# Kernel tuning notes

Hardware: AMD Instinct MI355X
Metric: run time of the kernel (lower is better)

Reference implementation:

```python
import jax, jax.numpy as jnp
import numpy as np

MULTIPLIER_N_BITS = 8
EPS = 1e-8


def setup_inputs() -> dict:
    key = jax.random.key(0)
    k1, k2, k3 = jax.random.split(key, 3)
    B, H, W, C, K = 16, 56, 56, 256, 16
    x = jax.random.normal(k1, (B, H, W, C), dtype=jnp.float32)
    # per-channel positive scales, typical activation-range magnitudes
    scales = jax.random.uniform(k2, (C,), dtype=jnp.float32, minval=0.1, maxval=2.0)
    # cluster centers live in the signed int domain [-2^(n-1), 2^(n-1)-1] of the multiplier
    cluster_centers = jax.random.uniform(k3, (K,), dtype=jnp.float32, minval=-128.0, maxval=127.0)
    return {"x": x, "scales": scales, "cluster_centers": cluster_centers}


def reference(x, scales, cluster_centers):
    mult = 2.0 ** (MULTIPLIER_N_BITS - 1)  # 128
    centers = jnp.round(cluster_centers)  # [K]
    # int_quantization_with_scale: clip(data/(scale+eps)*2^(n-1), -2^(n-1), 2^(n-1)-1)
    t = jnp.clip(x / (scales + EPS) * mult, -mult, mult - 1.0)  # [B,H,W,C]
    # nearest-center assignment over K centers ([...,K] intermediate)
    idx = jnp.argmin(jnp.abs(t[..., None] - centers), axis=-1)  # [B,H,W,C] int
    c = centers[idx]  # gather-dequant
    return c / mult * scales  # broadcast per-channel rescale
```

## Files before the change

kernel.cpp:

```cpp
#include <hip/hip_runtime.h>

#define NK 16
#define E  4

typedef float f32x4 __attribute__((ext_vector_type(4)));

__device__ __forceinline__ float argmin16(float t, const float* cen) {
    float best = 3.4e38f;
    float bc = 0.0f;
#pragma unroll
    for (int k = 0; k < NK; ++k) {
        float d = fabsf(t - cen[k]);
        bool p = d < best;
        best = p ? d : best;
        bc   = p ? cen[k] : bc;
    }
    return bc;
}

__global__ __launch_bounds__(256) void lutfq_kernel(
    const f32x4* __restrict__ x,
    const float* __restrict__ scales,
    const float* __restrict__ centers,
    f32x4*       __restrict__ out,
    int n4)
{
    __shared__ float s_lut[512];

    const int tid = threadIdx.x;
    const int i0 = blockIdx.x * (256 * E) + tid;

    f32x4 v[E];
#pragma unroll
    for (int u = 0; u < E; ++u) {
        int i = i0 + u * 256;
        v[u] = (i < n4) ? x[i] : f32x4{0.f, 0.f, 0.f, 0.f};
    }

    float cen[NK];
#pragma unroll
    for (int k = 0; k < NK; ++k) cen[k] = rintf(centers[k]);

    const int c4 = (tid & 63) * 4;
    const f32x4 sv = *reinterpret_cast<const f32x4*>(&scales[c4]);
    float den[4], r256[4], so[4];
#pragma unroll
    for (int j = 0; j < 4; ++j) {
        den[j]  = sv[j] + 1e-8f;
        r256[j] = 256.0f / den[j];
        so[j]   = sv[j] * 0.0078125f;
    }

    for (int ub = tid; ub < 512; ub += 256) {
        float t;
        if (ub == 0)        t = -128.0f;
        else if (ub >= 510) t = 127.0f;
        else                t = 0.5f * (float)(ub - 256) + 0.25f;
        s_lut[ub] = argmin16(t, cen);
    }
    __syncthreads();

    auto process = [&](f32x4 xv) -> f32x4 {
        f32x4 r;
#pragma unroll
        for (int j = 0; j < 4; ++j) {
            float u2 = xv[j] * r256[j];
            u2 = fminf(fmaxf(u2, -256.0f), 254.0f);

            float fl   = floorf(u2);
            float frac = u2 - fl;
            int   ub   = (int)fl + 256;

            float c = s_lut[ub];

            bool band = (frac < 0x1p-12f) | (frac > 1.0f - 0x1p-12f);
            bool rail = (u2 == -256.0f) | (u2 == 254.0f);
            if (band && !rail) {
                float t = (xv[j] / den[j]) * 128.0f;
                t = fminf(fmaxf(t, -128.0f), 127.0f);
                c = argmin16(t, cen);
            }
            r[j] = c * so[j];
        }
        return r;
    };

#pragma unroll
    for (int u = 0; u < E; ++u) {
        int i = i0 + u * 256;
        f32x4 r = process(v[u]);
        if (i < n4) __builtin_nontemporal_store(r, &out[i]);
    }
}

extern "C" void kernel_launch(void* const* d_in, const int* in_sizes, int n_in,
                              void* d_out, int out_size, void* d_ws, size_t ws_size,
                              hipStream_t stream) {
    const float* x       = (const float*)d_in[0];
    const float* scales  = (const float*)d_in[1];
    const float* centers = (const float*)d_in[2];
    float* out = (float*)d_out;

    int n4 = out_size / 4;
    int per_block = 256 * E;
    int blocks = (n4 + per_block - 1) / per_block;

    lutfq_kernel<<<blocks, 256, 0, stream>>>(
        (const f32x4*)x, scales, centers, (f32x4*)out, n4);
}
```

Measured before the change: 21.31 us.

## Precompute LUT and per-channel constants in a prep kernel via workspace

```diff
diff --git a/kernel.cpp b/kernel.cpp
--- a/kernel.cpp
+++ b/kernel.cpp
@@ -1,9 +1,16 @@
 #include <hip/hip_runtime.h>
 
 #define NK 16
-#define E  4
+#define E  7
 
-typedef float f32x4 __attribute__((ext_vector_type(4)));
+typedef float  f32x4 __attribute__((ext_vector_type(4)));
+typedef float  f32x2 __attribute__((ext_vector_type(2)));
+
+#define WS_LUT   0
+#define WS_CEN   512
+#define WS_DEN   528
+#define WS_R256  784
+#define WS_SO    1040
 
 __device__ __forceinline__ float argmin16(float t, const float* cen) {
     float best = 3.4e38f;
@@ -18,18 +25,51 @@
     return bc;
 }
 
-__global__ __launch_bounds__(256) void lutfq_kernel(
-    const f32x4* __restrict__ x,
+__global__ __launch_bounds__(256) void lutfq_prep(
     const float* __restrict__ scales,
     const float* __restrict__ centers,
+    float*       __restrict__ ws)
+{
+    const int tid = threadIdx.x;
+    float cen[NK];
+#pragma unroll
+    for (int k = 0; k < NK; ++k) cen[k] = rintf(centers[k]);
+    if (tid < NK) ws[WS_CEN + tid] = cen[tid];
+
+    float s   = scales[tid];
+    float den = s + 1e-8f;
+    ws[WS_DEN  + tid] = den;
+    ws[WS_R256 + tid] = 256.0f / den;
+    ws[WS_SO   + tid] = s * 0.0078125f;
+
+    for (int ub = tid; ub < 512; ub += 256) {
+        float t;
+        if (ub == 0)        t = -128.0f;
+        else if (ub >= 510) t = 127.0f;
+        else                t = 0.5f * (float)(ub - 256) + 0.25f;
+        ws[WS_LUT + ub] = argmin16(t, cen);
+    }
+}
+
+__global__ __launch_bounds__(256, 7) void lutfq_main(
+    const f32x4* __restrict__ x,
+    const float* __restrict__ ws,
     f32x4*       __restrict__ out,
     int n4)
 {
     __shared__ float s_lut[512];
+    __shared__ float s_cd[272];
 
     const int tid = threadIdx.x;
+
+    f32x2 lutv = *reinterpret_cast<const f32x2*>(&ws[WS_LUT + 2 * tid]);
+    float cdv  = ws[WS_CEN + tid];
+    float cdv2 = (tid < NK) ? ws[WS_CEN + 256 + tid] : 0.f;
+    const int c4 = (tid & 63) * 4;
+    f32x4 r256 = *reinterpret_cast<const f32x4*>(&ws[WS_R256 + c4]);
+    f32x4 so   = *reinterpret_cast<const f32x4*>(&ws[WS_SO   + c4]);
+
     const int i0 = blockIdx.x * (256 * E) + tid;
-
     f32x4 v[E];
 #pragma unroll
     for (int u = 0; u < E; ++u) {
@@ -37,30 +77,15 @@
         v[u] = (i < n4) ? x[i] : f32x4{0.f, 0.f, 0.f, 0.f};
     }
 
-    float cen[NK];
-#pragma unroll
-    for (int k = 0; k < NK; ++k) cen[k] = rintf(centers[k]);
-
-    const int c4 = (tid & 63) * 4;
-    const f32x4 sv = *reinterpret_cast<const f32x4*>(&scales[c4]);
-    float den[4], r256[4], so[4];
-#pragma unroll
-    for (int j = 0; j < 4; ++j) {
-        den[j]  = sv[j] + 1e-8f;
-        r256[j] = 256.0f / den[j];
-        so[j]   = sv[j] * 0.0078125f;
-    }
-
-    for (int ub = tid; ub < 512; ub += 256) {
-        float t;
-        if (ub == 0)        t = -128.0f;
-        else if (ub >= 510) t = 127.0f;
-        else                t = 0.5f * (float)(ub - 256) + 0.25f;
-        s_lut[ub] = argmin16(t, cen);
-    }
+    *reinterpret_cast<f32x2*>(&s_lut[2 * tid]) = lutv;
+    s_cd[tid] = cdv;
+    if (tid < NK) s_cd[256 + tid] = cdv2;
     __syncthreads();
 
-    auto process = [&](f32x4 xv) -> f32x4 {
+#pragma unroll
+    for (int u = 0; u < E; ++u) {
+        int i = i0 + u * 256;
+        f32x4 xv = v[u];
         f32x4 r;
 #pragma unroll
         for (int j = 0; j < 4; ++j) {
@@ -76,20 +101,14 @@
             bool band = (frac < 0x1p-12f) | (frac > 1.0f - 0x1p-12f);
             bool rail = (u2 == -256.0f) | (u2 == 254.0f);
             if (band && !rail) {
-                float t = (xv[j] / den[j]) * 128.0f;
+                float den = s_cd[16 + c4 + j];
+                float t = (xv[j] / den) * 128.0f;
                 t = fminf(fmaxf(t, -128.0f), 127.0f);
-                c = argmin16(t, cen);
+                c = argmin16(t, &s_cd[0]);
             }
             r[j] = c * so[j];
         }
-        return r;
-    };
-
-#pragma unroll
-    for (int u = 0; u < E; ++u) {
-        int i = i0 + u * 256;
-        f32x4 r = process(v[u]);
-        if (i < n4) __builtin_nontemporal_store(r, &out[i]);
+        if (i < n4) out[i] = r;
     }
 }
 
@@ -100,11 +119,13 @@
     const float* scales  = (const float*)d_in[1];
     const float* centers = (const float*)d_in[2];
     float* out = (float*)d_out;
+    float* ws  = (float*)d_ws;
 
     int n4 = out_size / 4;
     int per_block = 256 * E;
     int blocks = (n4 + per_block - 1) / per_block;
 
-    lutfq_kernel<<<blocks, 256, 0, stream>>>(
-        (const f32x4*)x, scales, centers, (f32x4*)out, n4);
+    lutfq_prep<<<1, 256, 0, stream>>>(scales, centers, ws);
+    lutfq_main<<<blocks, 256, 0, stream>>>(
+        (const f32x4*)x, ws, (f32x4*)out, n4);
 }
```

After: 27.68 us. 1.3x slower.
